# Optimization experiments

Hardware: AMD Instinct MI355X
Metric: run time of the kernel (lower is better)

The kernel has to match this reference:

```python
import jax, jax.numpy as jnp
import numpy as np

NUM_LAYERS = 2


def setup_inputs() -> dict:
    key = jax.random.key(0)
    k1, k2, k3, k4 = jax.random.split(key, 4)
    N, E, D = 50000, 800000, 100
    features = jax.random.normal(k1, (N, D), dtype=jnp.float32)
    # stacked nn.Linear weights, one [D,D] per layer (no bias)
    W = jax.random.normal(k2, (NUM_LAYERS, D, D), dtype=jnp.float32) * 0.02
    src = jax.random.randint(k3, (E,), 0, N)
    dst = jax.random.randint(k4, (E,), 0, N)
    return {"features": features, "W": W, "src": src, "dst": dst}


def reference(features, W, src, dst):
    N, D = features.shape
    num_layers = W.shape[0]
    inv_lp1 = 1.0 / (num_layers + 1)

    # --- graph preprocessing (mirrors ItemConv.graph setter) ---
    # add self loops (fill_diag 1.0), then row-normalize by inverse degree
    loop = jnp.arange(N)
    src_all = jnp.concatenate([src, loop])  # message sources
    dst_all = jnp.concatenate([dst, loop])  # message destinations (rows of adj_t)
    deg = jax.ops.segment_sum(
        jnp.ones(src_all.shape, dtype=features.dtype), dst_all, num_segments=N
    )
    deg_inv = jnp.where(deg > 0, 1.0 / deg, 0.0)
    w = deg_inv[dst_all]  # per-edge weight: row-normalized, [E+N]

    # --- forward (LightGCN-style conv with linear projections) ---
    avg = features * inv_lp1
    x = features
    for i in range(num_layers):
        x = x @ W[i].T  # nn.Linear(D, D, bias=False)
        # SpMM: out[d] = sum_{e: dst=d} w_e * x[src_e]
        x = jax.ops.segment_sum(w[:, None] * x[src_all], dst_all, num_segments=N)
        # F.normalize(x): L2 along dim=-1 with eps=1e-12 (max-clamped norm)
        norm = jnp.linalg.norm(x, axis=-1, keepdims=True)
        avg = avg + (x / jnp.maximum(norm, 1e-12)) * inv_lp1
    return avg
```

## Files before the change

### kernel.cpp

```cpp
#include <hip/hip_runtime.h>

#define D 100
#define YSTRIDE 128
#define BSHIFT 7
#define BSIZE 128
#define BMASK 127
#define NBKMAX 512
#define EPB 2048
#define DCAP 4096

typedef __attribute__((ext_vector_type(8))) short bf8v;
typedef __attribute__((ext_vector_type(4))) float f4v;

__device__ inline unsigned short f2bf(float f) {
    unsigned u = __float_as_uint(f);
    return (unsigned short)((u + 0x7fffu + ((u >> 16) & 1u)) >> 16);
}
__device__ inline float bflo(unsigned v) { return __uint_as_float(v << 16); }
__device__ inline float bfhi(unsigned v) { return __uint_as_float(v & 0xffff0000u); }
__device__ inline unsigned short pk8(float a, float b) {
    return (unsigned short)(__builtin_amdgcn_cvt_pk_fp8_f32(a, b, 0, false) & 0xffff);
}
__device__ inline float up8lo(unsigned v) { return __builtin_amdgcn_cvt_f32_fp8((int)v, 0); }
__device__ inline float up8hi(unsigned v) { return __builtin_amdgcn_cvt_f32_fp8((int)v, 1); }

__device__ inline void scan512_excl(int* a, int* t, int tid) {
    int v0 = a[2 * tid], v1 = a[2 * tid + 1];
    t[tid] = v0 + v1;
    __syncthreads();
    for (int off = 1; off < 256; off <<= 1) {
        int u = (tid >= off) ? t[tid - off] : 0;
        __syncthreads();
        t[tid] += u;
        __syncthreads();
    }
    int base = (tid ? t[tid - 1] : 0);
    a[2 * tid]     = base;
    a[2 * tid + 1] = base + v0;
    __syncthreads();
}

__global__ __launch_bounds__(256) void k_pack(const float* __restrict__ x0, unsigned* __restrict__ s8,
                                              int* __restrict__ bcnt, int N) {
    int t = blockIdx.x * 256 + threadIdx.x;
    if (t < NBKMAX) bcnt[t] = 0;
    if (t >= N * 32) return;
    int d = t >> 5, q = t & 31;
    unsigned p = 0u;
    if (q < D / 4) {
        float4 v = *(const float4*)(x0 + (long)d * D + q * 4);
        p = (unsigned)pk8(v.x, v.y) | ((unsigned)pk8(v.z, v.w) << 16);
    }
    s8[t] = p;
}

__global__ __launch_bounds__(256) void k_wc(const float* __restrict__ W, float* __restrict__ Wc) {
    int t = blockIdx.x * 256 + threadIdx.x;
    if (t >= D * D) return;
    int i = t / D, j = t - i * D;
    const float* w2 = W + D * D + (long)i * D;
    float s = 0.f;
    for (int k = 0; k < D; k++) s += w2[k] * W[(long)k * D + j];
    Wc[t] = s;
}

__global__ __launch_bounds__(256) void k_prep(const float* __restrict__ W1, const float* __restrict__ Wc,
                                              unsigned short* __restrict__ P, int wtot) {
    int t = blockIdx.x * 256 + threadIdx.x;
    if (t >= wtot) return;
    int lane = t & 63;
    int r = t >> 6;
    int kt = r & 3;
    int r2 = r >> 2;
    int nt = r2 % 7;
    int l  = r2 / 7;
    const float* M = (l == 0) ? W1 : Wc;
    int ng = nt * 16 + (lane & 15);
    int k0 = kt * 32 + (lane >> 4) * 8;
    unsigned short u[8];
#pragma unroll
    for (int j = 0; j < 8; j++) {
        int k = k0 + j;
        u[j] = (ng < D && k < D) ? f2bf(M[(long)ng * D + k]) : (unsigned short)0;
    }
    uint4 o;
    o.x = (unsigned)u[0] | ((unsigned)u[1] << 16);
    o.y = (unsigned)u[2] | ((unsigned)u[3] << 16);
    o.z = (unsigned)u[4] | ((unsigned)u[5] << 16);
    o.w = (unsigned)u[6] | ((unsigned)u[7] << 16);
    *(uint4*)(P + (long)t * 8) = o;
}

__global__ __launch_bounds__(256) void k_bucketA(const int* __restrict__ dst,
                                                 int* __restrict__ bucket_cnt, int E, int nbk) {
    __shared__ int lhist[NBKMAX];
    int tid = threadIdx.x;
    int base = blockIdx.x * EPB;
    int count = min(EPB, E - base);
    for (int i = tid; i < NBKMAX; i += 256) lhist[i] = 0;
    __syncthreads();
    for (int i = tid; i < count; i += 256) atomicAdd(&lhist[dst[base + i] >> BSHIFT], 1);
    __syncthreads();
    for (int b = tid; b < nbk; b += 256)
        if (lhist[b]) atomicAdd(&bucket_cnt[b], lhist[b]);
}

__global__ __launch_bounds__(256) void k_scanB(const int* __restrict__ bucket_cnt,
                                               int* __restrict__ bucket_off,
                                               int* __restrict__ bucket_cur, int nbk, int E) {
    __shared__ int a[NBKMAX], t[256];
    int tid = threadIdx.x;
    a[tid]       = (tid < nbk) ? bucket_cnt[tid] : 0;
    a[tid + 256] = (tid + 256 < nbk) ? bucket_cnt[tid + 256] : 0;
    __syncthreads();
    scan512_excl(a, t, tid);
    if (tid < nbk)       { bucket_off[tid] = a[tid];             bucket_cur[tid] = a[tid]; }
    if (tid + 256 < nbk) { bucket_off[tid + 256] = a[tid + 256]; bucket_cur[tid + 256] = a[tid + 256]; }
    if (tid == 0) bucket_off[nbk] = E;
}

__global__ __launch_bounds__(256) void k_bucketC(const int* __restrict__ src,
                                                 const int* __restrict__ dst,
                                                 int* __restrict__ bucket_cur,
                                                 unsigned* __restrict__ ebuf, int E, int nbk) {
    __shared__ int lhist[NBKMAX], lstart[NBKMAX], runS[NBKMAX], t[256];
    __shared__ unsigned stage[EPB];
    int tid = threadIdx.x;
    int base = blockIdx.x * EPB;
    int count = min(EPB, E - base);

    for (int i = tid; i < NBKMAX; i += 256) lhist[i] = 0;
    __syncthreads();
    for (int i = tid; i < count; i += 256) atomicAdd(&lhist[dst[base + i] >> BSHIFT], 1);
    __syncthreads();
    for (int i = tid; i < NBKMAX; i += 256) lstart[i] = lhist[i];
    __syncthreads();
    scan512_excl(lstart, t, tid);
    for (int b = tid; b < nbk; b += 256) {
        int c = lhist[b];
        runS[b] = c ? atomicAdd(&bucket_cur[b], c) : 0;
    }
    __syncthreads();
    for (int i = tid; i < NBKMAX; i += 256) lhist[i] = 0;
    __syncthreads();
    for (int i = tid; i < count; i += 256) {
        int dv = dst[base + i];
        int sv = src[base + i];
        int b = dv >> BSHIFT;
        int r = atomicAdd(&lhist[b], 1);
        stage[lstart[b] + r] = ((unsigned)(dv & BMASK) << 16) | (unsigned)sv;
    }
    __syncthreads();
    int wave = tid >> 6, lane = tid & 63;
    for (int b = wave; b < nbk; b += 4) {
        int c = lhist[b], ls = lstart[b], rs = runS[b];
        for (int j = lane; j < c; j += 64) ebuf[rs + j] = stage[ls + j];
    }
}

__global__ __launch_bounds__(256) void k_bucketD(const unsigned* __restrict__ ebuf,
                                                 const int* __restrict__ bucket_off,
                                                 int* __restrict__ col, int* __restrict__ rowptr,
                                                 int N, int nbk, int E) {
    __shared__ int lh[BSIZE], ls[BSIZE];
    __shared__ int colStage[DCAP];
    int b = blockIdx.x;
    int tid = threadIdx.x;
    int beg = bucket_off[b], end = bucket_off[b + 1];
    int cnt = end - beg;

    if (tid < BSIZE) lh[tid] = 0;
    __syncthreads();
    for (int i = tid; i < cnt; i += 256) atomicAdd(&lh[ebuf[beg + i] >> 16], 1);
    __syncthreads();
    if (tid < BSIZE) ls[tid] = lh[tid];
    __syncthreads();
    for (int off = 1; off < BSIZE; off <<= 1) {
        int v = (tid >= off && tid < BSIZE) ? ls[tid - off] : 0;
        __syncthreads();
        if (tid < BSIZE) ls[tid] += v;
        __syncthreads();
    }
    if (tid < BSIZE) ls[tid] -= lh[tid];
    __syncthreads();
    int d0 = b * BSIZE;
    if (tid < BSIZE && d0 + tid < N) rowptr[d0 + tid] = beg + ls[tid];
    if (b == nbk - 1 && tid == 0) rowptr[N] = E;
    if (tid < BSIZE) lh[tid] = 0;
    __syncthreads();
    if (cnt <= DCAP) {
        for (int i = tid; i < cnt; i += 256) {
            unsigned p = ebuf[beg + i];
            int r = p >> 16, s = (int)(p & 0xffffu);
            int k = atomicAdd(&lh[r], 1);
            colStage[ls[r] + k] = s;
        }
        __syncthreads();
        for (int i = tid; i < cnt; i += 256) col[beg + i] = colStage[i];
    } else {
        for (int i = tid; i < cnt; i += 256) {
            unsigned p = ebuf[beg + i];
            int r = p >> 16, s = (int)(p & 0xffffu);
            int k = atomicAdd(&lh[r], 1);
            col[beg + ls[r] + k] = s;
        }
    }
}

__global__ __launch_bounds__(256) void k_spmm(const unsigned short* __restrict__ g8,
                                              const int* __restrict__ rowptr,
                                              const int* __restrict__ col,
                                              const unsigned* __restrict__ self16,
                                              unsigned short* __restrict__ o8,
                                              unsigned* __restrict__ o16,
                                              int write8, int N) {
    int wave = threadIdx.x >> 6;
    int lane = threadIdx.x & 63;
    int d0 = (blockIdx.x * 4 + wave) * 2;
    if (d0 >= N) return;
    int d1 = d0 + 1;
    bool has1 = d1 < N;

    int b0 = __builtin_amdgcn_readfirstlane(rowptr[d0]);
    int e0 = __builtin_amdgcn_readfirstlane(rowptr[d0 + 1]);
    int e1 = has1 ? __builtin_amdgcn_readfirstlane(rowptr[d1 + 1]) : e0;

    float ax0, ay0, ax1, ay1;
    if (self16) {
        unsigned sv0 = self16[(long)d0 * 64 + lane];
        ax0 = bflo(sv0); ay0 = bfhi(sv0);
        unsigned sv1 = self16[(long)(has1 ? d1 : d0) * 64 + lane];
        ax1 = bflo(sv1); ay1 = bfhi(sv1);
    } else {
        unsigned sv0 = g8[(long)d0 * 64 + lane];
        ax0 = up8lo(sv0); ay0 = up8hi(sv0);
        unsigned sv1 = g8[(long)(has1 ? d1 : d0) * 64 + lane];
        ax1 = up8lo(sv1); ay1 = up8hi(sv1);
    }

    for (int win = b0; win < e1; win += 64) {
        int m = e1 - win;
        if (m > 64) m = 64;
        int c = col[win + lane];
        int j = 0;
        for (; j + 8 <= m; j += 8) {
            int s0 = __builtin_amdgcn_readlane(c, j);
            int s1 = __builtin_amdgcn_readlane(c, j + 1);
            int s2 = __builtin_amdgcn_readlane(c, j + 2);
            int s3 = __builtin_amdgcn_readlane(c, j + 3);
            int s4 = __builtin_amdgcn_readlane(c, j + 4);
            int s5 = __builtin_amdgcn_readlane(c, j + 5);
            int s6 = __builtin_amdgcn_readlane(c, j + 6);
            int s7 = __builtin_amdgcn_readlane(c, j + 7);
            unsigned v0 = g8[(long)s0 * 64 + lane];
            unsigned v1 = g8[(long)s1 * 64 + lane];
            unsigned v2 = g8[(long)s2 * 64 + lane];
            unsigned v3 = g8[(long)s3 * 64 + lane];
            unsigned v4 = g8[(long)s4 * 64 + lane];
            unsigned v5 = g8[(long)s5 * 64 + lane];
            unsigned v6 = g8[(long)s6 * 64 + lane];
            unsigned v7 = g8[(long)s7 * 64 + lane];
#pragma unroll
            for (int k = 0; k < 8; k++) {
                unsigned vv = (k == 0) ? v0 : (k == 1) ? v1 : (k == 2) ? v2 : (k == 3) ? v3
                            : (k == 4) ? v4 : (k == 5) ? v5 : (k == 6) ? v6 : v7;
                float w0 = (win + j + k < e0) ? 1.f : 0.f;
                float w1 = 1.f - w0;
                float lx = up8lo(vv), ly = up8hi(vv);
                ax0 += lx * w0; ay0 += ly * w0;
                ax1 += lx * w1; ay1 += ly * w1;
            }
        }
        for (; j < m; j++) {
            int s = __builtin_amdgcn_readlane(c, j);
            unsigned vv = g8[(long)s * 64 + lane];
            float w0 = (win + j < e0) ? 1.f : 0.f;
            float w1 = 1.f - w0;
            float lx = up8lo(vv), ly = up8hi(vv);
            ax0 += lx * w0; ay0 += ly * w0;
            ax1 += lx * w1; ay1 += ly * w1;
        }
    }

    float dinv0 = 1.f / (float)(e0 - b0 + 1);
    float dinv1 = 1.f / (float)(e1 - e0 + 1);
    float rx0 = ax0 * dinv0, ry0 = ay0 * dinv0;
    float rx1 = ax1 * dinv1, ry1 = ay1 * dinv1;

    bool act = lane < (D / 2);
    unsigned p0 = act ? ((unsigned)f2bf(rx0) | ((unsigned)f2bf(ry0) << 16)) : 0u;
    o16[(long)d0 * 64 + lane] = p0;
    if (write8) o8[(long)d0 * 64 + lane] = act ? pk8(rx0, ry0) : (unsigned short)0;
    if (has1) {
        unsigned p1 = act ? ((unsigned)f2bf(rx1) | ((unsigned)f2bf(ry1) << 16)) : 0u;
        o16[(long)d1 * 64 + lane] = p1;
        if (write8) o8[(long)d1 * 64 + lane] = act ? pk8(rx1, ry1) : (unsigned short)0;
    }
}

__global__ __launch_bounds__(256) void k_epi(const unsigned short* __restrict__ u16,
                                             const unsigned short* __restrict__ v16,
                                             const unsigned short* __restrict__ P,
                                             const float* __restrict__ x0,
                                             float invlp1, float* __restrict__ out, int N) {
    int wave = threadIdx.x >> 6;
    int lane = threadIdx.x & 63;
    int quad = lane >> 4;
    int l16  = lane & 15;
    int rowbase = (blockIdx.x * 4 + wave) * 16;
    if (rowbase >= N) return;
    int arow = rowbase + l16;
    if (arow >= N) arow = N - 1;

    bf8v aU[4], aV[4];
    const unsigned short* ur = u16 + (long)arow * YSTRIDE;
    const unsigned short* vr = v16 + (long)arow * YSTRIDE;
#pragma unroll
    for (int kt = 0; kt < 4; kt++) {
        int k0 = kt * 32 + quad * 8;
        union { bf8v v; uint4 u; } a, b;
        a.u = *(const uint4*)(ur + k0);
        b.u = *(const uint4*)(vr + k0);
        aU[kt] = a.v;
        aV[kt] = b.v;
    }

    f4v accU[7], accV[7];
#pragma unroll
    for (int nt = 0; nt < 7; nt++) { accU[nt] = (f4v){0,0,0,0}; accV[nt] = (f4v){0,0,0,0}; }

    const uint4* bp = (const uint4*)P;
#pragma unroll
    for (int nt = 0; nt < 7; nt++) {
#pragma unroll
        for (int kt = 0; kt < 4; kt++) {
            union { uint4 u; bf8v v; } b1, b2;
            b1.u = bp[(nt * 4 + kt) * 64 + lane];
            b2.u = bp[(28 + nt * 4 + kt) * 64 + lane];
            accU[nt] = __builtin_amdgcn_mfma_f32_16x16x32_bf16(aU[kt], b1.v, accU[nt], 0, 0, 0);
            accV[nt] = __builtin_amdgcn_mfma_f32_16x16x32_bf16(aV[kt], b2.v, accV[nt], 0, 0, 0);
        }
    }

    float sU[4], sV[4];
#pragma unroll
    for (int i = 0; i < 4; i++) {
        float nu = 0.f, nv = 0.f;
#pragma unroll
        for (int nt = 0; nt < 7; nt++) {
            nu += accU[nt][i] * accU[nt][i];
            nv += accV[nt][i] * accV[nt][i];
        }
#pragma unroll
        for (int m = 1; m < 16; m <<= 1) {
            nu += __shfl_xor(nu, m);
            nv += __shfl_xor(nv, m);
        }
        sU[i] = invlp1 / fmaxf(sqrtf(nu), 1e-12f);
        sV[i] = invlp1 / fmaxf(sqrtf(nv), 1e-12f);
    }

#pragma unroll
    for (int nt = 0; nt < 7; nt++) {
        int cc = nt * 16 + l16;
        if (cc < D) {
#pragma unroll
            for (int i = 0; i < 4; i++) {
                int rr = rowbase + quad * 4 + i;
                if (rr < N) {
                    long idx = (long)rr * D + cc;
                    out[idx] = x0[idx] * invlp1 + accU[nt][i] * sU[i] + accV[nt][i] * sV[i];
                }
            }
        }
    }
}


extern "C" void kernel_launch(void* const* d_in, const int* in_sizes, int n_in,
                              void* d_out, int out_size, void* d_ws, size_t ws_size,
                              hipStream_t stream) {
    const float* features = (const float*)d_in[0];
    const float* W        = (const float*)d_in[1];
    const int*   src      = (const int*)d_in[2];
    const int*   dstv     = (const int*)d_in[3];

    int N = in_sizes[0] / D;
    int E = in_sizes[2];
    int L = in_sizes[1] / (D * D);
    float invlp1 = 1.f / (float)(L + 1);
    int NBK = (N + BSIZE - 1) >> BSHIFT;

    char*  ws  = (char*)d_ws;
    size_t off = 0;
    auto alloc = [&](size_t bytes) -> void* {
        void* p = (void*)(ws + off);
        off += (bytes + 255) & ~(size_t)255;
        return p;
    };
    unsigned*       s8     = (unsigned*)alloc((size_t)N * 32 * sizeof(unsigned));
    unsigned*       u8     = (unsigned*)alloc((size_t)N * 32 * sizeof(unsigned));
    unsigned*       u16    = (unsigned*)alloc((size_t)N * 64 * sizeof(unsigned));
    unsigned*       v16    = (unsigned*)alloc((size_t)N * 64 * sizeof(unsigned));
    float*          Wc     = (float*)alloc((size_t)D * D * sizeof(float));
    unsigned short* wpack  = (unsigned short*)alloc((size_t)2 * 7 * 4 * 64 * 8 * sizeof(unsigned short));
    unsigned*       ebuf   = (unsigned*)alloc((size_t)E * sizeof(unsigned));
    int*            colb   = (int*)alloc((size_t)E * sizeof(int));
    int*            rowptr = (int*)alloc((size_t)(N + 1) * sizeof(int));
    int*            bcnt   = (int*)alloc((size_t)NBKMAX * sizeof(int));
    int*            boff   = (int*)alloc((size_t)(NBKMAX + 1) * sizeof(int));
    int*            bcur   = (int*)alloc((size_t)NBKMAX * sizeof(int));

    int nebk = (E + EPB - 1) / EPB;
    int wtot = 2 * 7 * 4 * 64;

    k_pack<<<(N * 32 + 255) / 256, 256, 0, stream>>>(features, s8, bcnt, N);
    k_wc<<<(D * D + 255) / 256, 256, 0, stream>>>(W, Wc);
    k_prep<<<(wtot + 255) / 256, 256, 0, stream>>>(W, Wc, wpack, wtot);
    k_bucketA<<<nebk, 256, 0, stream>>>(dstv, bcnt, E, NBK);
    k_scanB<<<1, 256, 0, stream>>>(bcnt, boff, bcur, NBK, E);
    k_bucketC<<<nebk, 256, 0, stream>>>(src, dstv, bcur, ebuf, E, NBK);
    k_bucketD<<<NBK, 256, 0, stream>>>(ebuf, boff, colb, rowptr, N, NBK, E);

    int spmmblocks = ((N + 1) / 2 + 3) / 4;
    k_spmm<<<spmmblocks, 256, 0, stream>>>((const unsigned short*)s8, rowptr, colb,
                                           (const unsigned*)nullptr,
                                           (unsigned short*)u8, u16, 1, N);
    k_spmm<<<spmmblocks, 256, 0, stream>>>((const unsigned short*)u8, rowptr, colb,
                                           u16, (unsigned short*)nullptr, v16, 0, N);

    int nrowtiles = (N + 15) / 16;
    int epiblocks = (nrowtiles + 3) / 4;
    k_epi<<<epiblocks, 256, 0, stream>>>((const unsigned short*)u16, (const unsigned short*)v16,
                                         wpack, features, invlp1, (float*)d_out, N);
}
```

Baseline: 215.5 us.

## Split feature dimension into halves for SpMM gathers and fuse preprocessing kernels

The fp8 gather table is stored as two separate 50-column halves, each with a 64-byte row. Each SpMM layer now runs as two passes, one per half, so each pass gathers from a smaller table that is more likely to stay resident in L2. Separately, the pack, weight-combine, weight-pack and bucket-histogram kernels are merged into one launch, with a memset replacing the in-kernel counter clear. In exchange, the SpMM launches double, the column and rowptr arrays are traversed twice, and only 25 of 64 lanes carry useful work in each wave.

```diff
diff --git a/kernel.cpp b/kernel.cpp
--- a/kernel.cpp
+++ b/kernel.cpp
@@ -40,69 +40,70 @@
     __syncthreads();
 }
 
-__global__ __launch_bounds__(256) void k_pack(const float* __restrict__ x0, unsigned* __restrict__ s8,
-                                              int* __restrict__ bcnt, int N) {
-    int t = blockIdx.x * 256 + threadIdx.x;
-    if (t < NBKMAX) bcnt[t] = 0;
-    if (t >= N * 32) return;
-    int d = t >> 5, q = t & 31;
-    unsigned p = 0u;
-    if (q < D / 4) {
-        float4 v = *(const float4*)(x0 + (long)d * D + q * 4);
-        p = (unsigned)pk8(v.x, v.y) | ((unsigned)pk8(v.z, v.w) << 16);
-    }
-    s8[t] = p;
-}
-
-__global__ __launch_bounds__(256) void k_wc(const float* __restrict__ W, float* __restrict__ Wc) {
-    int t = blockIdx.x * 256 + threadIdx.x;
-    if (t >= D * D) return;
-    int i = t / D, j = t - i * D;
-    const float* w2 = W + D * D + (long)i * D;
-    float s = 0.f;
-    for (int k = 0; k < D; k++) s += w2[k] * W[(long)k * D + j];
-    Wc[t] = s;
-}
-
-__global__ __launch_bounds__(256) void k_prep(const float* __restrict__ W1, const float* __restrict__ Wc,
-                                              unsigned short* __restrict__ P, int wtot) {
-    int t = blockIdx.x * 256 + threadIdx.x;
-    if (t >= wtot) return;
-    int lane = t & 63;
-    int r = t >> 6;
-    int kt = r & 3;
-    int r2 = r >> 2;
-    int nt = r2 % 7;
-    int l  = r2 / 7;
-    const float* M = (l == 0) ? W1 : Wc;
-    int ng = nt * 16 + (lane & 15);
-    int k0 = kt * 32 + (lane >> 4) * 8;
-    unsigned short u[8];
-#pragma unroll
-    for (int j = 0; j < 8; j++) {
-        int k = k0 + j;
-        u[j] = (ng < D && k < D) ? f2bf(M[(long)ng * D + k]) : (unsigned short)0;
-    }
-    uint4 o;
-    o.x = (unsigned)u[0] | ((unsigned)u[1] << 16);
-    o.y = (unsigned)u[2] | ((unsigned)u[3] << 16);
-    o.z = (unsigned)u[4] | ((unsigned)u[5] << 16);
-    o.w = (unsigned)u[6] | ((unsigned)u[7] << 16);
-    *(uint4*)(P + (long)t * 8) = o;
-}
-
-__global__ __launch_bounds__(256) void k_bucketA(const int* __restrict__ dst,
-                                                 int* __restrict__ bucket_cnt, int E, int nbk) {
+__global__ __launch_bounds__(256) void k_pre(const float* __restrict__ x0, const float* __restrict__ W,
+                                             unsigned* __restrict__ s8, unsigned short* __restrict__ P,
+                                             int* __restrict__ bcnt, const int* __restrict__ dst,
+                                             int N, int E, int nbk, int packb, int ablk) {
     __shared__ int lhist[NBKMAX];
     int tid = threadIdx.x;
-    int base = blockIdx.x * EPB;
-    int count = min(EPB, E - base);
-    for (int i = tid; i < NBKMAX; i += 256) lhist[i] = 0;
-    __syncthreads();
-    for (int i = tid; i < count; i += 256) atomicAdd(&lhist[dst[base + i] >> BSHIFT], 1);
-    __syncthreads();
-    for (int b = tid; b < nbk; b += 256)
-        if (lhist[b]) atomicAdd(&bucket_cnt[b], lhist[b]);
+    int bx = blockIdx.x;
+
+    if (bx < packb) {
+        int t = bx * 256 + tid;
+        if (t >= N * 32) return;
+        int node = t >> 5, q = t & 31;
+        int half = q >> 4, qi = q & 15;
+        float f[4];
+#pragma unroll
+        for (int j = 0; j < 4; j++) {
+            int dd = 4 * qi + j;
+            f[j] = (dd < 50) ? x0[(long)node * D + half * 50 + dd] : 0.f;
+        }
+        unsigned p = (unsigned)pk8(f[0], f[1]) | ((unsigned)pk8(f[2], f[3]) << 16);
+        s8[((long)half * N + node) * 16 + qi] = p;
+    } else if (bx < packb + ablk) {
+        int base = (bx - packb) * EPB;
+        int count = min(EPB, E - base);
+        for (int i = tid; i < NBKMAX; i += 256) lhist[i] = 0;
+        __syncthreads();
+        for (int i = tid; i < count; i += 256) atomicAdd(&lhist[dst[base + i] >> BSHIFT], 1);
+        __syncthreads();
+        for (int b = tid; b < nbk; b += 256)
+            if (lhist[b]) atomicAdd(&bcnt[b], lhist[b]);
+    } else {
+        int t = (bx - packb - ablk) * 256 + tid;
+        int wtot = 2 * 7 * 4 * 64;
+        if (t >= wtot) return;
+        int lane = t & 63;
+        int r = t >> 6;
+        int kt = r & 3;
+        int r2 = r >> 2;
+        int nt = r2 % 7;
+        int l  = r2 / 7;
+        int ng = nt * 16 + (lane & 15);
+        int k0 = kt * 32 + (lane >> 4) * 8;
+        unsigned short u[8];
+#pragma unroll
+        for (int j = 0; j < 8; j++) {
+            int k = k0 + j;
+            float mv = 0.f;
+            if (ng < D && k < D) {
+                if (l == 0) {
+                    mv = W[(long)ng * D + k];
+                } else {
+                    const float* w2 = W + D * D + (long)ng * D;
+                    for (int kk = 0; kk < D; kk++) mv += w2[kk] * W[(long)kk * D + k];
+                }
+            }
+            u[j] = f2bf(mv);
+        }
+        uint4 o;
+        o.x = (unsigned)u[0] | ((unsigned)u[1] << 16);
+        o.y = (unsigned)u[2] | ((unsigned)u[3] << 16);
+        o.z = (unsigned)u[4] | ((unsigned)u[5] << 16);
+        o.w = (unsigned)u[6] | ((unsigned)u[7] << 16);
+        *(uint4*)(P + (long)t * 8) = o;
+    }
 }
 
 __global__ __launch_bounds__(256) void k_scanB(const int* __restrict__ bucket_cnt,
@@ -207,15 +208,16 @@
     }
 }
 
-__global__ __launch_bounds__(256) void k_spmm(const unsigned short* __restrict__ g8,
-                                              const int* __restrict__ rowptr,
-                                              const int* __restrict__ col,
-                                              const unsigned* __restrict__ self16,
-                                              unsigned short* __restrict__ o8,
-                                              unsigned* __restrict__ o16,
-                                              int write8, int N) {
+__global__ __launch_bounds__(256) void k_spmm_h(const unsigned short* __restrict__ g8h,
+                                                const int* __restrict__ rowptr,
+                                                const int* __restrict__ col,
+                                                const unsigned* __restrict__ self16,
+                                                unsigned short* __restrict__ o8h,
+                                                unsigned* __restrict__ o16,
+                                                int h, int N) {
     int wave = threadIdx.x >> 6;
     int lane = threadIdx.x & 63;
+    int leff = (lane < 25) ? lane : 24;
     int d0 = (blockIdx.x * 4 + wave) * 2;
     if (d0 >= N) return;
     int d1 = d0 + 1;
@@ -227,14 +229,14 @@
 
     float ax0, ay0, ax1, ay1;
     if (self16) {
-        unsigned sv0 = self16[(long)d0 * 64 + lane];
+        unsigned sv0 = self16[(long)d0 * 64 + h * 25 + leff];
         ax0 = bflo(sv0); ay0 = bfhi(sv0);
-        unsigned sv1 = self16[(long)(has1 ? d1 : d0) * 64 + lane];
+        unsigned sv1 = self16[(long)(has1 ? d1 : d0) * 64 + h * 25 + leff];
         ax1 = bflo(sv1); ay1 = bfhi(sv1);
     } else {
-        unsigned sv0 = g8[(long)d0 * 64 + lane];
+        unsigned sv0 = g8h[(long)d0 * 32 + leff];
         ax0 = up8lo(sv0); ay0 = up8hi(sv0);
-        unsigned sv1 = g8[(long)(has1 ? d1 : d0) * 64 + lane];
+        unsigned sv1 = g8h[(long)(has1 ? d1 : d0) * 32 + leff];
         ax1 = up8lo(sv1); ay1 = up8hi(sv1);
     }
 
@@ -252,14 +254,14 @@
             int s5 = __builtin_amdgcn_readlane(c, j + 5);
             int s6 = __builtin_amdgcn_readlane(c, j + 6);
             int s7 = __builtin_amdgcn_readlane(c, j + 7);
-            unsigned v0 = g8[(long)s0 * 64 + lane];
-            unsigned v1 = g8[(long)s1 * 64 + lane];
-            unsigned v2 = g8[(long)s2 * 64 + lane];
-            unsigned v3 = g8[(long)s3 * 64 + lane];
-            unsigned v4 = g8[(long)s4 * 64 + lane];
-            unsigned v5 = g8[(long)s5 * 64 + lane];
-            unsigned v6 = g8[(long)s6 * 64 + lane];
-            unsigned v7 = g8[(long)s7 * 64 + lane];
+            unsigned v0 = g8h[(long)s0 * 32 + leff];
+            unsigned v1 = g8h[(long)s1 * 32 + leff];
+            unsigned v2 = g8h[(long)s2 * 32 + leff];
+            unsigned v3 = g8h[(long)s3 * 32 + leff];
+            unsigned v4 = g8h[(long)s4 * 32 + leff];
+            unsigned v5 = g8h[(long)s5 * 32 + leff];
+            unsigned v6 = g8h[(long)s6 * 32 + leff];
+            unsigned v7 = g8h[(long)s7 * 32 + leff];
 #pragma unroll
             for (int k = 0; k < 8; k++) {
                 unsigned vv = (k == 0) ? v0 : (k == 1) ? v1 : (k == 2) ? v2 : (k == 3) ? v3
@@ -273,7 +275,7 @@
         }
         for (; j < m; j++) {
             int s = __builtin_amdgcn_readlane(c, j);
-            unsigned vv = g8[(long)s * 64 + lane];
+            unsigned vv = g8h[(long)s * 32 + leff];
             float w0 = (win + j < e0) ? 1.f : 0.f;
             float w1 = 1.f - w0;
             float lx = up8lo(vv), ly = up8hi(vv);
@@ -287,14 +289,16 @@
     float rx0 = ax0 * dinv0, ry0 = ay0 * dinv0;
     float rx1 = ax1 * dinv1, ry1 = ay1 * dinv1;
 
-    bool act = lane < (D / 2);
-    unsigned p0 = act ? ((unsigned)f2bf(rx0) | ((unsigned)f2bf(ry0) << 16)) : 0u;
-    o16[(long)d0 * 64 + lane] = p0;
-    if (write8) o8[(long)d0 * 64 + lane] = act ? pk8(rx0, ry0) : (unsigned short)0;
-    if (has1) {
-        unsigned p1 = act ? ((unsigned)f2bf(rx1) | ((unsigned)f2bf(ry1) << 16)) : 0u;
-        o16[(long)d1 * 64 + lane] = p1;
-        if (write8) o8[(long)d1 * 64 + lane] = act ? pk8(rx1, ry1) : (unsigned short)0;
+    if (lane < 25) {
+        o16[(long)d0 * 64 + h * 25 + lane] = (unsigned)f2bf(rx0) | ((unsigned)f2bf(ry0) << 16);
+        if (o8h) o8h[(long)d0 * 32 + lane] = pk8(rx0, ry0);
+        if (has1) {
+            o16[(long)d1 * 64 + h * 25 + lane] = (unsigned)f2bf(rx1) | ((unsigned)f2bf(ry1) << 16);
+            if (o8h) o8h[(long)d1 * 32 + lane] = pk8(rx1, ry1);
+        }
+    } else if (h == 1 && lane < 39) {
+        o16[(long)d0 * 64 + 25 + lane] = 0u;
+        if (has1) o16[(long)d1 * 64 + 25 + lane] = 0u;
     }
 }
 
@@ -398,11 +402,10 @@
         off += (bytes + 255) & ~(size_t)255;
         return p;
     };
-    unsigned*       s8     = (unsigned*)alloc((size_t)N * 32 * sizeof(unsigned));
-    unsigned*       u8     = (unsigned*)alloc((size_t)N * 32 * sizeof(unsigned));
+    unsigned*       s8     = (unsigned*)alloc((size_t)2 * N * 16 * sizeof(unsigned));
+    unsigned*       u8     = (unsigned*)alloc((size_t)2 * N * 16 * sizeof(unsigned));
     unsigned*       u16    = (unsigned*)alloc((size_t)N * 64 * sizeof(unsigned));
     unsigned*       v16    = (unsigned*)alloc((size_t)N * 64 * sizeof(unsigned));
-    float*          Wc     = (float*)alloc((size_t)D * D * sizeof(float));
     unsigned short* wpack  = (unsigned short*)alloc((size_t)2 * 7 * 4 * 64 * 8 * sizeof(unsigned short));
     unsigned*       ebuf   = (unsigned*)alloc((size_t)E * sizeof(unsigned));
     int*            colb   = (int*)alloc((size_t)E * sizeof(int));
@@ -411,23 +414,32 @@
     int*            boff   = (int*)alloc((size_t)(NBKMAX + 1) * sizeof(int));
     int*            bcur   = (int*)alloc((size_t)NBKMAX * sizeof(int));
 
-    int nebk = (E + EPB - 1) / EPB;
-    int wtot = 2 * 7 * 4 * 64;
-
-    k_pack<<<(N * 32 + 255) / 256, 256, 0, stream>>>(features, s8, bcnt, N);
-    k_wc<<<(D * D + 255) / 256, 256, 0, stream>>>(W, Wc);
-    k_prep<<<(wtot + 255) / 256, 256, 0, stream>>>(W, Wc, wpack, wtot);
-    k_bucketA<<<nebk, 256, 0, stream>>>(dstv, bcnt, E, NBK);
+    int nebk  = (E + EPB - 1) / EPB;
+    int wtot  = 2 * 7 * 4 * 64;
+    int packb = (N * 32 + 255) / 256;
+    int pblk  = (wtot + 255) / 256;
+
+    hipMemsetAsync(bcnt, 0, (size_t)NBK * sizeof(int), stream);
+    k_pre<<<packb + nebk + pblk, 256, 0, stream>>>(features, W, s8, wpack, bcnt, dstv,
+                                                   N, E, NBK, packb, nebk);
     k_scanB<<<1, 256, 0, stream>>>(bcnt, boff, bcur, NBK, E);
     k_bucketC<<<nebk, 256, 0, stream>>>(src, dstv, bcur, ebuf, E, NBK);
     k_bucketD<<<NBK, 256, 0, stream>>>(ebuf, boff, colb, rowptr, N, NBK, E);
 
-    int spmmblocks = ((N + 1) / 2 + 3) / 4;
-    k_spmm<<<spmmblocks, 256, 0, stream>>>((const unsigned short*)s8, rowptr, colb,
-                                           (const unsigned*)nullptr,
-                                           (unsigned short*)u8, u16, 1, N);
-    k_spmm<<<spmmblocks, 256, 0, stream>>>((const unsigned short*)u8, rowptr, colb,
-                                           u16, (unsigned short*)nullptr, v16, 0, N);
+    int spmmblocks = (N + 7) / 8;
+    const unsigned short* s8h0 = (const unsigned short*)s8;
+    const unsigned short* s8h1 = (const unsigned short*)(s8 + (size_t)N * 16);
+    unsigned short*       u8h0 = (unsigned short*)u8;
+    unsigned short*       u8h1 = (unsigned short*)(u8 + (size_t)N * 16);
+
+    k_spmm_h<<<spmmblocks, 256, 0, stream>>>(s8h0, rowptr, colb, (const unsigned*)nullptr,
+                                             u8h0, u16, 0, N);
+    k_spmm_h<<<spmmblocks, 256, 0, stream>>>(u8h0, rowptr, colb, u16,
+                                             (unsigned short*)nullptr, v16, 0, N);
+    k_spmm_h<<<spmmblocks, 256, 0, stream>>>(s8h1, rowptr, colb, (const unsigned*)nullptr,
+                                             u8h1, u16, 1, N);
+    k_spmm_h<<<spmmblocks, 256, 0, stream>>>(u8h1, rowptr, colb, u16,
+                                             (unsigned short*)nullptr, v16, 1, N);
 
     int nrowtiles = (N + 15) / 16;
     int epiblocks = (nrowtiles + 3) / 4;
```

New measurement: 285.6 us. +32.5%, slower.
